# Optimization experiments

Measured on AMD Instinct MI355X. Metric: run time of the kernel, lower is better.

The kernel has to match this reference:

```python
import jax, jax.numpy as jnp
import numpy as np

B, V, H = 4, 256, 128
BN_EPS = 1e-5


def setup_inputs() -> dict:
    key = jax.random.key(0)
    ks = jax.random.split(key, 20)
    n = lambda k, shape, s=1.0: jax.random.normal(k, shape, dtype=jnp.float32) * s
    return {
        "h": n(ks[0], (B, V, H)),
        "e": n(ks[1], (B, V, V, H)),
        "x": jax.random.uniform(ks[2], (B, V, 2), dtype=jnp.float32),
        "graph": jax.random.randint(ks[3], (B, V, V), 0, 2, dtype=jnp.int32),
        "Uw": n(ks[4], (H, H), 0.05), "Ub": n(ks[5], (H,), 0.05),
        "Vw": n(ks[6], (H, H), 0.05), "Vb": n(ks[7], (H,), 0.05),
        "Aw": n(ks[8], (H, H), 0.05), "Ab": n(ks[9], (H,), 0.05),
        "Bw": n(ks[10], (H, H), 0.05), "Bb": n(ks[11], (H,), 0.05),
        "Cw": n(ks[12], (H, H), 0.05), "Cb": n(ks[13], (H,), 0.05),
        "dw": n(ks[14], (H, 1), 0.05), "db": n(ks[15], (H,), 0.05),
        "ew": n(ks[16], (1, H), 0.05), "eb": n(ks[17], (1,), 0.05),
        "c": n(ks[18], (1,), 0.1),
        "gamma_h": jnp.ones((H,), jnp.float32), "beta_h": jnp.zeros((H,), jnp.float32),
        "gamma_e": jnp.ones((H,), jnp.float32), "beta_e": jnp.zeros((H,), jnp.float32),
    }


def _batchnorm(z, gamma, beta):
    # BatchNorm1d over flattened leading dims (batch statistics, biased var)
    zf = z.reshape(-1, z.shape[-1])
    mu = zf.mean(0)
    var = zf.var(0)
    return (z - mu) * jax.lax.rsqrt(var + BN_EPS) * gamma + beta


def reference(h, e, x, graph, Uw, Ub, Vw, Vb, Aw, Ab, Bw, Bb, Cw, Cb,
              dw, db, ew, eb, c, gamma_h, beta_h, gamma_e, beta_e):
    lin = lambda z, W, b: jnp.einsum('...i,oi->...o', z, W) + b
    Uh = lin(h, Uw, Ub)                      # B V H
    Vh = lin(h, Vw, Vb)                      # B V H (node-j features)
    Ah = lin(h, Aw, Ab)
    Bh = lin(h, Bw, Bb)
    Ce = lin(e, Cw, Cb)                      # B V V H

    # diff[b,i,j] = x_i - x_j  (== x_to - x_from in the torch code)
    diff = x[:, :, None, :] - x[:, None, :, :]          # B V V 2
    d2 = jnp.sum(diff * diff, axis=-1, keepdims=True)   # B V V 1
    dist = jnp.where(d2 > 0, jnp.sqrt(jnp.where(d2 > 0, d2, 1.0)), 0.0)

    # e_ij = Ah_j + Bh_i + Ce_ij + d(|x_i - x_j|)
    e_new = Ah[:, None, :, :] + Bh[:, :, None, :] + Ce + dist * dw[:, 0] + db
    gates = jax.nn.sigmoid(e_new)                        # B V V H
    pa = jax.nn.sigmoid(jnp.einsum('bijh,oh->bijo', e_new, ew) + eb)  # B V V 1

    x_upd = c * jnp.sum(pa * diff, axis=2)               # B V 2

    # aggregate: zero out where graph == 1 (disconnected), sum over j
    msg = jnp.where(graph[..., None] == 1, 0.0, gates * Vh[:, None, :, :])
    h_new = Uh + jnp.sum(msg, axis=2)                    # B V H

    h_new = jax.nn.relu(_batchnorm(h_new, gamma_h, beta_h))
    e_out = jax.nn.relu(_batchnorm(e_new, gamma_e, beta_e))

    return (h + h_new, e + e_out, x + x_upd)
```

## Files before the change

kernel.cpp:

```cpp
#include <hip/hip_runtime.h>
#include <math.h>

#define BB 4
#define VV 256
#define HH 128
#define NBI (BB*VV)
#define NE  (NBI*VV)
#define BN_EPS 1e-5f

typedef _Float16 half8_ __attribute__((ext_vector_type(8)));
typedef float    floatx4 __attribute__((ext_vector_type(4)));

__device__ __forceinline__ float sigmoidf_(float v) {
    return 1.0f / (1.0f + __expf(-v));
}

__device__ __forceinline__ unsigned pk(float x, float y) {
    auto h = __builtin_amdgcn_cvt_pkrtz(x, y);
    return __builtin_bit_cast(unsigned, h);
}

__device__ __forceinline__ float h2f(unsigned short u) {
    _Float16 h = __builtin_bit_cast(_Float16, u);
    return (float)h;
}

__global__ __launch_bounds__(128)
void k1_lin4(const float* __restrict__ h,
             const float* __restrict__ Uw, const float* __restrict__ Ub,
             const float* __restrict__ Vw, const float* __restrict__ Vb,
             const float* __restrict__ Aw, const float* __restrict__ Ab,
             const float* __restrict__ Bw, const float* __restrict__ Bb,
             const float* __restrict__ Cw,
             float* __restrict__ Uh, float* __restrict__ Vh,
             float* __restrict__ Ah, float* __restrict__ Bh,
             unsigned short* __restrict__ cwp)
{
    __shared__ float sh[HH];
    int bi = blockIdx.x;
    int o  = threadIdx.x;

    if (bi < 128) {
        int idx  = bi*128 + o;
        int j    = idx & 7;
        int slot = idx >> 3;
        int lane = slot & 63;
        int tile = slot >> 6;
        int ht   = tile & 7;
        int ks   = tile >> 3;
        int k    = ks*32 + (lane >> 4)*8 + j;
        int hh   = ht*16 + (lane & 15);
        _Float16 hv = (_Float16)Cw[hh*HH + k];
        cwp[idx] = __builtin_bit_cast(unsigned short, hv);
    }

    sh[o] = h[bi*HH + o];
    __syncthreads();

    float su = Ub[o], sv = Vb[o], sa = Ab[o], sb = Bb[o];
    const float4* sh4 = (const float4*)sh;
    const float4* Uw4 = (const float4*)Uw;
    const float4* Vw4 = (const float4*)Vw;
    const float4* Aw4 = (const float4*)Aw;
    const float4* Bw4 = (const float4*)Bw;
    #pragma unroll 8
    for (int k4 = 0; k4 < 32; ++k4) {
        float4 hv = sh4[k4];
        float4 wu = Uw4[o*32 + k4];
        float4 wv = Vw4[o*32 + k4];
        float4 wa = Aw4[o*32 + k4];
        float4 wb = Bw4[o*32 + k4];
        su += hv.x*wu.x + hv.y*wu.y + hv.z*wu.z + hv.w*wu.w;
        sv += hv.x*wv.x + hv.y*wv.y + hv.z*wv.z + hv.w*wv.w;
        sa += hv.x*wa.x + hv.y*wa.y + hv.z*wa.z + hv.w*wa.w;
        sb += hv.x*wb.x + hv.y*wb.y + hv.z*wb.z + hv.w*wb.w;
    }
    Uh[bi*HH + o] = su;
    Vh[bi*HH + o] = sv;
    Ah[bi*HH + o] = sa;
    Bh[bi*HH + o] = sb;
}

__global__ __launch_bounds__(256, 4)
void k2_main(const float* __restrict__ e,
             const float* __restrict__ x,
             const int*   __restrict__ graph,
             const unsigned short* __restrict__ cwp,
             const float* __restrict__ Cb,
             const float* __restrict__ dw, const float* __restrict__ db,
             const float* __restrict__ ew, const float* __restrict__ ebp,
             const float* __restrict__ Uh, const float* __restrict__ Vh,
             const float* __restrict__ Ah, const float* __restrict__ Bh,
             uint4* __restrict__ stash,
             float* __restrict__ epart,
             float* __restrict__ hacc,
             float* __restrict__ xupd)
{
    __shared__ unsigned short s_b[16384];
    __shared__ float s_dist[256], s_dx[256], s_dy[256];
    __shared__ int   s_g[256];
    __shared__ float s_red[4*HH];

    int tid  = threadIdx.x;
    int bi   = blockIdx.x;
    int b    = bi >> 8;
    int lane = tid & 63;
    int w    = tid >> 6;
    int hl   = lane & 15;
    int q    = lane >> 4;

    {
        const int4* src = (const int4*)cwp;
        int4* dst = (int4*)s_b;
        #pragma unroll
        for (int it = 0; it < 8; ++it) dst[tid + it*256] = src[tid + it*256];
    }

    float xi0 = x[bi*2 + 0], xi1 = x[bi*2 + 1];
    {
        int j = tid;
        float xj0 = x[(b*VV + j)*2 + 0], xj1 = x[(b*VV + j)*2 + 1];
        float dx = xi0 - xj0, dy = xi1 - xj1;
        float d2 = dx*dx + dy*dy;
        s_dx[j] = dx; s_dy[j] = dy;
        s_dist[j] = (d2 > 0.f) ? sqrtf(d2) : 0.f;
        s_g[j] = graph[(size_t)bi*VV + j];
    }

    float pre[8], dwv[8], ewv[8];
    #pragma unroll
    for (int ht = 0; ht < 8; ++ht) {
        int hh = ht*16 + hl;
        pre[ht] = Bh[bi*HH + hh] + Cb[hh] + db[hh];
        dwv[ht] = dw[hh];
        ewv[ht] = ew[hh];
    }
    float ebv = ebp[0];

    __syncthreads();

    float ssum[8] = {0,0,0,0,0,0,0,0};
    float ssq [8] = {0,0,0,0,0,0,0,0};
    float hsum[8] = {0,0,0,0,0,0,0,0};
    float xa0 = 0.f, xa1 = 0.f;

    #pragma unroll
    for (int ch = 0; ch < 4; ++ch) {
        int chunk = ch >> 1, half = ch & 1;
        int j0 = chunk*128 + w*32 + half*16;
        const float* eA = e + ((size_t)bi*VV + j0 + hl)*HH + q*8;

        float4 L[8];
        #pragma unroll
        for (int ks = 0; ks < 4; ++ks) {
            L[2*ks]   = *(const float4*)(eA + ks*32);
            L[2*ks+1] = *(const float4*)(eA + ks*32 + 4);
        }

        floatx4 acc[8];
        #pragma unroll
        for (int ht = 0; ht < 8; ++ht) acc[ht] = (floatx4){0.f,0.f,0.f,0.f};

        #pragma unroll
        for (int ks = 0; ks < 4; ++ks) {
            union { half8_ h; unsigned u[4]; } a;
            a.u[0] = pk(L[2*ks].x,   L[2*ks].y);
            a.u[1] = pk(L[2*ks].z,   L[2*ks].w);
            a.u[2] = pk(L[2*ks+1].x, L[2*ks+1].y);
            a.u[3] = pk(L[2*ks+1].z, L[2*ks+1].w);
            #pragma unroll
            for (int ht = 0; ht < 8; ++ht) {
                half8_ bf = *(const half8_*)(s_b + ((size_t)((ks*8 + ht)*64 + lane))*8);
                acc[ht] = __builtin_amdgcn_mfma_f32_16x16x32_f16(a.h, bf, acc[ht], 0, 0, 0);
            }
        }

        int jb = j0 + q*4;
        #pragma unroll
        for (int u = 0; u < 4; ++u) {
            int j = jb + u;
            const float* ap = Ah + ((size_t)(b*VV) + j)*HH + hl;
            const float* vp = Vh + ((size_t)(b*VV) + j)*HH + hl;
            float Av[8], Vv[8];
            #pragma unroll
            for (int ht = 0; ht < 8; ++ht) { Av[ht] = ap[ht*16]; Vv[ht] = vp[ht*16]; }

            float dist = s_dist[j], dx = s_dx[j], dy = s_dy[j];
            int g = s_g[j];

            float en[8];
            float padot = 0.f;
            #pragma unroll
            for (int ht = 0; ht < 8; ++ht) {
                float v = acc[ht][u] + Av[ht] + pre[ht] + dist*dwv[ht];
                en[ht] = v;
                ssum[ht] += v;
                ssq[ht]  += v*v;
                padot    += v*ewv[ht];
            }
            if (g != 1) {
                #pragma unroll
                for (int ht = 0; ht < 8; ++ht)
                    hsum[ht] += sigmoidf_(en[ht]) * Vv[ht];
            }

            uint4 st;
            st.x = pk(en[0], en[1]);
            st.y = pk(en[2], en[3]);
            st.z = pk(en[4], en[5]);
            st.w = pk(en[6], en[7]);
            stash[((size_t)bi*VV + j)*32 + hl] = st;

            padot += __shfl_xor(padot, 1);
            padot += __shfl_xor(padot, 2);
            padot += __shfl_xor(padot, 4);
            padot += __shfl_xor(padot, 8);
            if (hl == 0) {
                float pa = sigmoidf_(padot + ebv);
                xa0 += pa * dx;
                xa1 += pa * dy;
            }
        }
    }

    #pragma unroll
    for (int ht = 0; ht < 8; ++ht) {
        ssum[ht] += __shfl_xor(ssum[ht], 16); ssum[ht] += __shfl_xor(ssum[ht], 32);
        ssq[ht]  += __shfl_xor(ssq[ht],  16); ssq[ht]  += __shfl_xor(ssq[ht],  32);
        hsum[ht] += __shfl_xor(hsum[ht], 16); hsum[ht] += __shfl_xor(hsum[ht], 32);
    }

    __syncthreads();
    if (lane < 16) {
        #pragma unroll
        for (int ht = 0; ht < 8; ++ht) s_red[w*HH + ht*16 + lane] = ssum[ht];
    }
    __syncthreads();
    if (tid < HH)
        epart[(size_t)bi*2*HH + tid] =
            s_red[tid] + s_red[HH + tid] + s_red[2*HH + tid] + s_red[3*HH + tid];
    __syncthreads();
    if (lane < 16) {
        #pragma unroll
        for (int ht = 0; ht < 8; ++ht) s_red[w*HH + ht*16 + lane] = ssq[ht];
    }
    __syncthreads();
    if (tid < HH)
        epart[(size_t)bi*2*HH + HH + tid] =
            s_red[tid] + s_red[HH + tid] + s_red[2*HH + tid] + s_red[3*HH + tid];
    __syncthreads();
    if (lane < 16) {
        #pragma unroll
        for (int ht = 0; ht < 8; ++ht) s_red[w*HH + ht*16 + lane] = hsum[ht];
    }
    __syncthreads();
    if (tid < HH)
        hacc[bi*HH + tid] = Uh[bi*HH + tid] +
            s_red[tid] + s_red[HH + tid] + s_red[2*HH + tid] + s_red[3*HH + tid];
    __syncthreads();
    if (hl == 0) { s_red[w*4 + q] = xa0; s_red[16 + w*4 + q] = xa1; }
    __syncthreads();
    if (tid == 0) {
        float sx = 0.f, sy = 0.f;
        #pragma unroll
        for (int t = 0; t < 16; ++t) { sx += s_red[t]; sy += s_red[16 + t]; }
        xupd[bi*2 + 0] = sx;
        xupd[bi*2 + 1] = sy;
    }
}

__global__ __launch_bounds__(256)
void k3_stats(const float* __restrict__ epart, const float* __restrict__ hacc,
              const float* __restrict__ gamma_e, const float* __restrict__ beta_e,
              const float* __restrict__ gamma_h, const float* __restrict__ beta_h,
              float* __restrict__ coefs)
{
    __shared__ float rs[256], rq[256];
    int c = blockIdx.x, tid = threadIdx.x;
    float s = 0, q = 0;
    if (c < HH) {
        for (int r = tid; r < NBI; r += 256) {
            s += epart[(size_t)r*2*HH + c];
            q += epart[(size_t)r*2*HH + HH + c];
        }
    } else {
        int hh = c - HH;
        for (int r = tid; r < NBI; r += 256) {
            float v = hacc[r*HH + hh];
            s += v; q += v*v;
        }
    }
    rs[tid] = s; rq[tid] = q;
    __syncthreads();
    for (int off = 128; off > 0; off >>= 1) {
        if (tid < off) { rs[tid] += rs[tid+off]; rq[tid] += rq[tid+off]; }
        __syncthreads();
    }
    if (tid == 0) {
        float n = (c < HH) ? (float)NE : (float)NBI;
        float mean = rs[0] / n;
        float var  = rq[0] / n - mean*mean;
        int hh; float g, be;
        if (c < HH) { hh = c;      g = gamma_e[hh]; be = beta_e[hh]; }
        else        { hh = c - HH; g = gamma_h[hh]; be = beta_h[hh]; }
        float scale = g * rsqrtf(var + BN_EPS);
        float shift = be - mean*scale;
        if (c < HH) { coefs[hh]        = scale; coefs[HH + hh]   = shift; }
        else        { coefs[2*HH + hh] = scale; coefs[3*HH + hh] = shift; }
    }
}

__global__ __launch_bounds__(256)
void k4_eout(const float* __restrict__ e, const float* __restrict__ coefs,
             const float* __restrict__ h, const float* __restrict__ x,
             const float* __restrict__ hacc, const float* __restrict__ xupd,
             const float* __restrict__ cp,
             float* __restrict__ out0, float* __restrict__ out2,
             float* __restrict__ out1)
{
    __shared__ unsigned short s_t[64*144];
    int tid = threadIdx.x;
    int gid = blockIdx.x*256 + tid;
    if (gid < NBI*HH) {
        int hh = gid & 127;
        float v = hacc[gid]*coefs[2*HH + hh] + coefs[3*HH + hh];
        out0[gid] = h[gid] + fmaxf(v, 0.f);
        if (gid < NBI*2) out2[gid] = x[gid] + cp[0]*xupd[gid];
    }

    size_t r0 = (size_t)blockIdx.x * 64;
    const uint4* sp = (const uint4*)out1;
    #pragma unroll
    for (int it = 0; it < 4; ++it) {
        int rr = it*16 + (tid >> 4);
        int sg = tid & 15;
        *(uint4*)(s_t + rr*144 + sg*8) = sp[(r0 + rr)*32 + sg];
    }
    __syncthreads();

    const float4* e4  = (const float4*)e;
    float4* o4        = (float4*)out1;
    const float4* sc4 = (const float4*)coefs;
    const float4* sh4 = (const float4*)(coefs + HH);
    #pragma unroll
    for (int k = 0; k < 8; ++k) {
        int f  = k*256 + tid;
        int r  = f >> 5;
        int c4 = f & 31;
        size_t gi = (r0 + r)*32 + c4;
        float4 ev = e4[gi];
        float4 sc = sc4[c4], sh = sh4[c4];
        const unsigned short* row = s_t + r*144;
        int cc = c4*4;
        int pb = (cc & 15)*8 + (cc >> 4);
        float4 en;
        en.x = h2f(row[pb]);
        en.y = h2f(row[pb + 8]);
        en.z = h2f(row[pb + 16]);
        en.w = h2f(row[pb + 24]);
        float4 rr;
        rr.x = ev.x + fmaxf(en.x*sc.x + sh.x, 0.f);
        rr.y = ev.y + fmaxf(en.y*sc.y + sh.y, 0.f);
        rr.z = ev.z + fmaxf(en.z*sc.z + sh.z, 0.f);
        rr.w = ev.w + fmaxf(en.w*sc.w + sh.w, 0.f);
        o4[gi] = rr;
    }
}

extern "C" void kernel_launch(void* const* d_in, const int* in_sizes, int n_in,
                              void* d_out, int out_size, void* d_ws, size_t ws_size,
                              hipStream_t stream)
{
    (void)in_sizes; (void)n_in; (void)out_size; (void)ws_size;
    const float* h     = (const float*)d_in[0];
    const float* e     = (const float*)d_in[1];
    const float* x     = (const float*)d_in[2];
    const int*   graph = (const int*)d_in[3];
    const float* Uw = (const float*)d_in[4];
    const float* Ub = (const float*)d_in[5];
    const float* Vw = (const float*)d_in[6];
    const float* Vb = (const float*)d_in[7];
    const float* Aw = (const float*)d_in[8];
    const float* Ab = (const float*)d_in[9];
    const float* Bw = (const float*)d_in[10];
    const float* Bbv = (const float*)d_in[11];
    const float* Cw = (const float*)d_in[12];
    const float* Cb = (const float*)d_in[13];
    const float* dw = (const float*)d_in[14];
    const float* db = (const float*)d_in[15];
    const float* ew = (const float*)d_in[16];
    const float* eb = (const float*)d_in[17];
    const float* c  = (const float*)d_in[18];
    const float* gamma_h = (const float*)d_in[19];
    const float* beta_h  = (const float*)d_in[20];
    const float* gamma_e = (const float*)d_in[21];
    const float* beta_e  = (const float*)d_in[22];

    float* out0 = (float*)d_out;
    float* out1 = out0 + NBI*HH;
    float* out2 = out1 + (size_t)NE*HH;

    float* ws    = (float*)d_ws;
    float* Uh    = ws;
    float* Vh    = Uh + NBI*HH;
    float* Ah    = Vh + NBI*HH;
    float* Bh    = Ah + NBI*HH;
    float* hacc  = Bh + NBI*HH;
    float* epart = hacc + NBI*HH;
    float* xupd  = epart + (size_t)NBI*2*HH;
    float* coefs = xupd + NBI*2;
    unsigned short* cwp = (unsigned short*)(coefs + 4*HH);

    k1_lin4<<<NBI, 128, 0, stream>>>(h, Uw, Ub, Vw, Vb, Aw, Ab, Bw, Bbv, Cw,
                                     Uh, Vh, Ah, Bh, cwp);
    k2_main<<<NBI, 256, 0, stream>>>(e, x, graph, cwp, Cb, dw, db, ew, eb,
                                     Uh, Vh, Ah, Bh, (uint4*)out1,
                                     epart, hacc, xupd);
    k3_stats<<<2*HH, 256, 0, stream>>>(epart, hacc, gamma_e, beta_e,
                                       gamma_h, beta_h, coefs);
    k4_eout<<<NE/64, 256, 0, stream>>>(e, coefs, h, x, hacc, xupd, c,
                                       out0, out2, out1);
}
```

Measured before the change: 459.4 us.

## Prefetch next e chunk in k2, batch stash stores, use nontemporal memory ops

The main edge kernel now software-pipelines its loads. It issues the global loads of e for the next j chunk while the current chunk's epilogue runs, and it hoists half of the Ah/Vh loads ahead of that epilogue. The fp16 stash stores are gathered into registers and written with nontemporal stores after each chunk. The output kernel reads the stash and writes the final edge output with nontemporal loads and stores to reduce cache pollution. Holding the prefetched data needs more registers, so launch_bounds drops from 4 to 2 blocks per SIMD, which lowers occupancy.

```diff
diff --git a/kernel.cpp b/kernel.cpp
--- a/kernel.cpp
+++ b/kernel.cpp
@@ -10,6 +10,7 @@
 
 typedef _Float16 half8_ __attribute__((ext_vector_type(8)));
 typedef float    floatx4 __attribute__((ext_vector_type(4)));
+typedef unsigned uintx4  __attribute__((ext_vector_type(4)));
 
 __device__ __forceinline__ float sigmoidf_(float v) {
     return 1.0f / (1.0f + __expf(-v));
@@ -81,7 +82,7 @@
     Bh[bi*HH + o] = sb;
 }
 
-__global__ __launch_bounds__(256, 4)
+__global__ __launch_bounds__(256, 2)
 void k2_main(const float* __restrict__ e,
              const float* __restrict__ x,
              const int*   __restrict__ graph,
@@ -91,7 +92,7 @@
              const float* __restrict__ ew, const float* __restrict__ ebp,
              const float* __restrict__ Uh, const float* __restrict__ Vh,
              const float* __restrict__ Ah, const float* __restrict__ Bh,
-             uint4* __restrict__ stash,
+             uintx4* __restrict__ stash,
              float* __restrict__ epart,
              float* __restrict__ hacc,
              float* __restrict__ xupd)
@@ -144,18 +145,20 @@
     float hsum[8] = {0,0,0,0,0,0,0,0};
     float xa0 = 0.f, xa1 = 0.f;
 
+    float4 L[8];
+    {
+        const float* eA = e + ((size_t)bi*VV + w*32 + hl)*HH + q*8;
+        #pragma unroll
+        for (int ks = 0; ks < 4; ++ks) {
+            L[2*ks]   = *(const float4*)(eA + ks*32);
+            L[2*ks+1] = *(const float4*)(eA + ks*32 + 4);
+        }
+    }
+
     #pragma unroll
     for (int ch = 0; ch < 4; ++ch) {
         int chunk = ch >> 1, half = ch & 1;
         int j0 = chunk*128 + w*32 + half*16;
-        const float* eA = e + ((size_t)bi*VV + j0 + hl)*HH + q*8;
-
-        float4 L[8];
-        #pragma unroll
-        for (int ks = 0; ks < 4; ++ks) {
-            L[2*ks]   = *(const float4*)(eA + ks*32);
-            L[2*ks+1] = *(const float4*)(eA + ks*32 + 4);
-        }
 
         floatx4 acc[8];
         #pragma unroll
@@ -176,14 +179,44 @@
         }
 
         int jb = j0 + q*4;
+
+        float Avh[2][8], Vvh[2][8];
+        #pragma unroll
+        for (int u = 0; u < 2; ++u) {
+            const float* ap = Ah + ((size_t)(b*VV) + jb + u)*HH + hl;
+            const float* vp = Vh + ((size_t)(b*VV) + jb + u)*HH + hl;
+            #pragma unroll
+            for (int ht = 0; ht < 8; ++ht) {
+                Avh[u][ht] = ap[ht*16];
+                Vvh[u][ht] = vp[ht*16];
+            }
+        }
+
+        if (ch < 3) {
+            int chn = ch + 1;
+            int j0n = (chn >> 1)*128 + w*32 + (chn & 1)*16;
+            const float* eA = e + ((size_t)bi*VV + j0n + hl)*HH + q*8;
+            #pragma unroll
+            for (int ks = 0; ks < 4; ++ks) {
+                L[2*ks]   = *(const float4*)(eA + ks*32);
+                L[2*ks+1] = *(const float4*)(eA + ks*32 + 4);
+            }
+        }
+
+        uintx4 st[4];
         #pragma unroll
         for (int u = 0; u < 4; ++u) {
             int j = jb + u;
-            const float* ap = Ah + ((size_t)(b*VV) + j)*HH + hl;
-            const float* vp = Vh + ((size_t)(b*VV) + j)*HH + hl;
             float Av[8], Vv[8];
-            #pragma unroll
-            for (int ht = 0; ht < 8; ++ht) { Av[ht] = ap[ht*16]; Vv[ht] = vp[ht*16]; }
+            if (u < 2) {
+                #pragma unroll
+                for (int ht = 0; ht < 8; ++ht) { Av[ht] = Avh[u][ht]; Vv[ht] = Vvh[u][ht]; }
+            } else {
+                const float* ap = Ah + ((size_t)(b*VV) + j)*HH + hl;
+                const float* vp = Vh + ((size_t)(b*VV) + j)*HH + hl;
+                #pragma unroll
+                for (int ht = 0; ht < 8; ++ht) { Av[ht] = ap[ht*16]; Vv[ht] = vp[ht*16]; }
+            }
 
             float dist = s_dist[j], dx = s_dx[j], dy = s_dy[j];
             int g = s_g[j];
@@ -204,12 +237,10 @@
                     hsum[ht] += sigmoidf_(en[ht]) * Vv[ht];
             }
 
-            uint4 st;
-            st.x = pk(en[0], en[1]);
-            st.y = pk(en[2], en[3]);
-            st.z = pk(en[4], en[5]);
-            st.w = pk(en[6], en[7]);
-            stash[((size_t)bi*VV + j)*32 + hl] = st;
+            st[u].x = pk(en[0], en[1]);
+            st[u].y = pk(en[2], en[3]);
+            st[u].z = pk(en[4], en[5]);
+            st[u].w = pk(en[6], en[7]);
 
             padot += __shfl_xor(padot, 1);
             padot += __shfl_xor(padot, 2);
@@ -221,6 +252,11 @@
                 xa1 += pa * dy;
             }
         }
+
+        #pragma unroll
+        for (int u = 0; u < 4; ++u)
+            __builtin_nontemporal_store(st[u],
+                &stash[((size_t)bi*VV + jb + u)*32 + hl]);
     }
 
     #pragma unroll
@@ -329,17 +365,18 @@
     }
 
     size_t r0 = (size_t)blockIdx.x * 64;
-    const uint4* sp = (const uint4*)out1;
+    const uintx4* sp = (const uintx4*)out1;
     #pragma unroll
     for (int it = 0; it < 4; ++it) {
         int rr = it*16 + (tid >> 4);
         int sg = tid & 15;
-        *(uint4*)(s_t + rr*144 + sg*8) = sp[(r0 + rr)*32 + sg];
+        uintx4 v = __builtin_nontemporal_load(&sp[(r0 + rr)*32 + sg]);
+        *(uintx4*)(s_t + rr*144 + sg*8) = v;
     }
     __syncthreads();
 
     const float4* e4  = (const float4*)e;
-    float4* o4        = (float4*)out1;
+    floatx4* o4       = (floatx4*)out1;
     const float4* sc4 = (const float4*)coefs;
     const float4* sh4 = (const float4*)(coefs + HH);
     #pragma unroll
@@ -358,12 +395,12 @@
         en.y = h2f(row[pb + 8]);
         en.z = h2f(row[pb + 16]);
         en.w = h2f(row[pb + 24]);
-        float4 rr;
+        floatx4 rr;
         rr.x = ev.x + fmaxf(en.x*sc.x + sh.x, 0.f);
         rr.y = ev.y + fmaxf(en.y*sc.y + sh.y, 0.f);
         rr.z = ev.z + fmaxf(en.z*sc.z + sh.z, 0.f);
         rr.w = ev.w + fmaxf(en.w*sc.w + sh.w, 0.f);
-        o4[gi] = rr;
+        __builtin_nontemporal_store(rr, &o4[gi]);
     }
 }
 
@@ -414,7 +451,7 @@
     k1_lin4<<<NBI, 128, 0, stream>>>(h, Uw, Ub, Vw, Vb, Aw, Ab, Bw, Bbv, Cw,
                                      Uh, Vh, Ah, Bh, cwp);
     k2_main<<<NBI, 256, 0, stream>>>(e, x, graph, cwp, Cb, dw, db, ew, eb,
-                                     Uh, Vh, Ah, Bh, (uint4*)out1,
+                                     Uh, Vh, Ah, Bh, (uintx4*)out1,
                                      epart, hacc, xupd);
     k3_stats<<<2*HH, 256, 0, stream>>>(epart, hacc, gamma_e, beta_e,
                                        gamma_h, beta_h, coefs);
```

New measurement: 386.7 us. 1.19x faster.
